# Kernel tuning notes

Hardware: AMD Instinct MI355X
Metric: run time of the kernel (lower is better)

## Reference

```python
import jax, jax.numpy as jnp
import numpy as np

B, H, W = 8, 512, 512
KSIZE = 11   # HVS Gaussian kernel size
SIGMA = 2.0
EPS = 1e-8


def _gauss_kernel():
    ax = jnp.arange(KSIZE, dtype=jnp.float32) - (KSIZE - 1) / 2.0
    g = jnp.exp(-(ax ** 2) / (2.0 * SIGMA ** 2))
    k = jnp.outer(g, g)
    return k / jnp.sum(k)


def _conv_same(x, k):
    # x: (B,1,H,W), k: (kh,kw) symmetric -> conv == correlation
    return jax.lax.conv_general_dilated(
        x, k[None, None, :, :], window_strides=(1, 1), padding='SAME',
        dimension_numbers=('NCHW', 'OIHW', 'NCHW'))


def setup_inputs() -> dict:
    key = jax.random.key(0)
    k1, k2, k3 = jax.random.split(key, 3)
    prob_map = jax.random.uniform(k1, (B, 1, H, W), dtype=jnp.float32,
                                  minval=0.01, maxval=0.99)
    c = jax.random.uniform(k2, (B, 1, H, W), dtype=jnp.float32)
    # binary halftone sampled per-pixel from prob_map
    h_sampled = (jax.random.uniform(k3, (B, 1, H, W)) < prob_map).astype(jnp.float32)
    return {"prob_map": prob_map, "c": c, "h_sampled": h_sampled}


def reference(prob_map, c, h_sampled):
    k = _gauss_kernel()
    # perceived error of the sampled halftone: e = G*h - c
    e = _conv_same(h_sampled, k) - c                     # (B,1,H,W)
    corr = _conv_same(e, k)                              # (G*e), G symmetric
    sum_k2 = jnp.sum(k * k)
    delta = 1.0 - 2.0 * h_sampled                        # flip change per pixel
    # reward_calc.compute_reward_with_flip, vectorized over all pixels:
    # E(flip at a) - E = 2*delta_a*(G*e)(a) + delta_a^2 * sum(G^2)
    reward = 2.0 * delta * corr + (delta ** 2) * sum_k2  # >0 means flip hurts
    log_prob = jnp.where(h_sampled > 0.5,
                         jnp.log(prob_map + EPS),
                         jnp.log(1.0 - prob_map + EPS))
    # local expected-gradient (REINFORCE) loss, averaged over batch
    loss = -jnp.sum(reward * log_prob) / prob_map.shape[0]
    return loss
```

## Files before the change

kernel.cpp:

```cpp
#include <hip/hip_runtime.h>

typedef float v2f __attribute__((ext_vector_type(2)));
typedef float v4f __attribute__((ext_vector_type(4)));

#define IMG 512
#define TS  32
#define TPB 2
#define NBLK 1024

#define A_STR  58
#define BT_STR 46
#define ET_STR 44
#define CT_STR 36

__device__ __forceinline__ v2f lo2(v4f v) { return __builtin_shufflevector(v, v, 0, 1); }
__device__ __forceinline__ v2f hi2(v4f v) { return __builtin_shufflevector(v, v, 2, 3); }

__device__ __forceinline__ v4f ldq(const float* __restrict__ hmap, size_t base,
                                   int x0, int y0, int idx) {
    int r = idx / 14, q = idx - r * 14;
    int gy = y0 - 10 + r, gx0 = x0 - 12 + 4 * q;
    v4f v = {0.f, 0.f, 0.f, 0.f};
    if ((unsigned)gy < IMG) {
        const float* hr = &hmap[base + ((size_t)gy << 9)];
        if (gx0 >= 0 && gx0 + 3 < IMG) {
            v = *(const v4f*)&hr[gx0];
        } else {
            if ((unsigned)(gx0 + 0) < IMG) v.x = hr[gx0 + 0];
            if ((unsigned)(gx0 + 1) < IMG) v.y = hr[gx0 + 1];
            if ((unsigned)(gx0 + 2) < IMG) v.z = hr[gx0 + 2];
            if ((unsigned)(gx0 + 3) < IMG) v.w = hr[gx0 + 3];
        }
    }
    return v;
}

__global__ __launch_bounds__(256, 4) void marl_fused(
    const float* __restrict__ prob,
    const float* __restrict__ cmap,
    const float* __restrict__ hmap,
    float* __restrict__ out)
{
    __shared__ __align__(16) float Abuf[52 * A_STR];
    __shared__ __align__(16) float Bbuf[56 * BT_STR];
    __shared__ float red[4];

    const float W[11] = {0.00881223f, 0.02714358f, 0.06511405f, 0.12164908f,
                         0.17699840f, 0.20056540f, 0.17699840f, 0.12164908f,
                         0.06511405f, 0.02714358f, 0.00881223f};
    v2f wv[11];
#pragma unroll
    for (int i = 0; i < 11; ++i) wv[i] = (v2f){W[i], W[i]};
    float w2 = 0.f;
#pragma unroll
    for (int i = 0; i < 11; ++i) w2 += W[i] * W[i];
    const float sumk2 = w2 * w2;
    const v2f z = {0.f, 0.f};

    const int tid = threadIdx.x;
    const int i0 = tid, i1 = tid + 256, i2 = tid + 512;
    const int T0 = blockIdx.x * TPB;

    const int p1run = tid % 7, p1q = tid / 7;
    const int p2p = tid % 21, p2eq = tid / 21;
    const int p3oyq = tid & 3, p3ex = tid >> 2;
    const int oy0e = 2 * (tid & 15), ox0 = 2 * (tid >> 4);

    v2f hv[TPB][2], pv[TPB][2];
    float creg[TPB][2][4];

    {
        const int b = T0 >> 8, r8 = T0 & 255;
        const int x0 = (r8 & 15) * TS, y0 = (r8 >> 4) * TS;
        const size_t base = (size_t)b << 18;
        v4f ha = ldq(hmap, base, x0, y0, i0);
        v4f hb = ldq(hmap, base, x0, y0, i1);
        v4f hc = (tid < 216) ? ldq(hmap, base, x0, y0, i2) : (v4f){0.f,0.f,0.f,0.f};
        if (tid < 231) {
#pragma unroll
            for (int h = 0; h < 2; ++h) {
                int gy = y0 - 5 + 2 * p2p + h;
#pragma unroll
                for (int c = 0; c < 4; ++c) {
                    int gx = x0 - 5 + 4 * p2eq + c;
                    creg[0][h][c] = ((unsigned)gy < IMG && (unsigned)gx < IMG)
                        ? cmap[base + ((size_t)gy << 9) + gx] : 0.f;
                }
            }
        }
#pragma unroll
        for (int h = 0; h < 2; ++h) {
            size_t rowb = base + ((size_t)(y0 + oy0e + h) << 9) + (x0 + ox0);
            hv[0][h] = *(const v2f*)&hmap[rowb];
            pv[0][h] = *(const v2f*)&prob[rowb];
        }
        { int r = i0 / 14, q = i0 - r * 14; *(v4f*)&Abuf[r * A_STR + 4 * q] = ha; }
        { int r = i1 / 14, q = i1 - r * 14; *(v4f*)&Abuf[r * A_STR + 4 * q] = hb; }
        if (tid < 216) { int r = i2 / 14, q = i2 - r * 14; *(v4f*)&Abuf[r * A_STR + 4 * q] = hc; }
    }
    __syncthreads();

    float partial = 0.f;
    v4f pfh0, pfh1, pfh2;

#pragma unroll
    for (int t = 0; t < TPB; ++t) {
        const int T = T0 + t;
        const int r8 = T & 255;
        const int x0 = (r8 & 15) * TS, y0 = (r8 >> 4) * TS;

        if (tid < 98) {
            int by0 = 6 * p1run;
            v2f accLo[6] = {z, z, z, z, z, z}, accHi[6] = {z, z, z, z, z, z};
#pragma unroll
            for (int i = 0; i < 16; ++i) {
                v4f a = *(const v4f*)&Abuf[(by0 + i) * A_STR + 4 * p1q];
                v2f lo = lo2(a), hi = hi2(a);
#pragma unroll
                for (int r = 0; r < 6; ++r) {
                    int j = i - r;
                    if (j >= 0 && j < 11) { accLo[r] += wv[j] * lo; accHi[r] += wv[j] * hi; }
                }
            }
#pragma unroll
            for (int r = 0; r < 6; ++r) {
                int by = by0 + r;
                Bbuf[(4 * p1q + 0) * BT_STR + by] = accLo[r].x;
                Bbuf[(4 * p1q + 1) * BT_STR + by] = accLo[r].y;
                Bbuf[(4 * p1q + 2) * BT_STR + by] = accHi[r].x;
                Bbuf[(4 * p1q + 3) * BT_STR + by] = accHi[r].y;
            }
        }
        __syncthreads();

        if (tid < 231) {
            int ex0 = 4 * p2eq, ey0 = 2 * p2p;
            v2f acc[4] = {z, z, z, z};
#pragma unroll
            for (int i = 0; i < 14; ++i) {
                v2f bb = *(const v2f*)&Bbuf[(ex0 + 2 + i) * BT_STR + ey0];
#pragma unroll
                for (int c = 0; c < 4; ++c) {
                    int j = i - c;
                    if (j >= 0 && j < 11) acc[c] += wv[j] * bb;
                }
            }
#pragma unroll
            for (int c = 0; c < 4; ++c) {
                int ex = ex0 + c;
                if (ex < 42) {
                    int gx = x0 - 5 + ex;
                    bool xin = (unsigned)gx < IMG;
#pragma unroll
                    for (int h = 0; h < 2; ++h) {
                        int gy = y0 - 5 + ey0 + h;
                        float v = 0.f;
                        if (xin && (unsigned)gy < IMG)
                            v = acc[c][h] - creg[t][h][c];
                        Abuf[ex * ET_STR + ey0 + h] = v;
                    }
                }
            }
        }
        __syncthreads();

        if (t + 1 < TPB) {
            const int Tn = T + 1;
            const int nb = Tn >> 8, nr8 = Tn & 255;
            const int nx0 = (nr8 & 15) * TS, ny0 = (nr8 >> 4) * TS;
            const size_t nbase = (size_t)nb << 18;
            pfh0 = ldq(hmap, nbase, nx0, ny0, i0);
            pfh1 = ldq(hmap, nbase, nx0, ny0, i1);
            if (tid < 216) pfh2 = ldq(hmap, nbase, nx0, ny0, i2);
            if (tid < 231) {
#pragma unroll
                for (int h = 0; h < 2; ++h) {
                    int gy = ny0 - 5 + 2 * p2p + h;
#pragma unroll
                    for (int c = 0; c < 4; ++c) {
                        int gx = nx0 - 5 + 4 * p2eq + c;
                        creg[t + 1][h][c] = ((unsigned)gy < IMG && (unsigned)gx < IMG)
                            ? cmap[nbase + ((size_t)gy << 9) + gx] : 0.f;
                    }
                }
            }
#pragma unroll
            for (int h = 0; h < 2; ++h) {
                size_t rowb = nbase + ((size_t)(ny0 + oy0e + h) << 9) + (nx0 + ox0);
                hv[t + 1][h] = *(const v2f*)&hmap[rowb];
                pv[t + 1][h] = *(const v2f*)&prob[rowb];
            }
        }
        if (tid < 168) {
            int oy0 = 8 * p3oyq;
            const float* src = &Abuf[p3ex * ET_STR + oy0];
            v4f w0 = *(const v4f*)&src[0];
            v4f w1 = *(const v4f*)&src[4];
            v4f w2_ = *(const v4f*)&src[8];
            v4f w3 = *(const v4f*)&src[12];
            v4f w4 = *(const v4f*)&src[16];
            float win[20];
            *(v4f*)&win[0] = w0; *(v4f*)&win[4] = w1; *(v4f*)&win[8] = w2_;
            *(v4f*)&win[12] = w3; *(v4f*)&win[16] = w4;
            float o[8];
#pragma unroll
            for (int k = 0; k < 8; ++k) {
                float acc = 0.f;
#pragma unroll
                for (int j = 0; j < 11; ++j) acc += W[j] * win[k + j];
                o[k] = acc;
            }
            *(v4f*)&Bbuf[p3ex * CT_STR + oy0]     = (v4f){o[0], o[1], o[2], o[3]};
            *(v4f*)&Bbuf[p3ex * CT_STR + oy0 + 4] = (v4f){o[4], o[5], o[6], o[7]};
        }
        __syncthreads();

        if (t + 1 < TPB) {
            { int r = i0 / 14, q = i0 - r * 14; *(v4f*)&Abuf[r * A_STR + 4 * q] = pfh0; }
            { int r = i1 / 14, q = i1 - r * 14; *(v4f*)&Abuf[r * A_STR + 4 * q] = pfh1; }
            if (tid < 216) { int r = i2 / 14, q = i2 - r * 14; *(v4f*)&Abuf[r * A_STR + 4 * q] = pfh2; }
        }
        {
            v2f acc[2] = {z, z};
#pragma unroll
            for (int i = 0; i < 12; ++i) {
                v2f ct = *(const v2f*)&Bbuf[(ox0 + i) * CT_STR + oy0e];
#pragma unroll
                for (int c = 0; c < 2; ++c) {
                    int j = i - c;
                    if (j >= 0 && j < 11) acc[c] += wv[j] * ct;
                }
            }
#pragma unroll
            for (int h = 0; h < 2; ++h) {
#pragma unroll
                for (int c = 0; c < 2; ++c) {
                    float h_ = hv[t][h][c], p_ = pv[t][h][c];
                    float logp = __logf(h_ > 0.5f ? p_ + 1e-8f : 1.f - p_ + 1e-8f);
                    float delta = 1.f - 2.f * h_;
                    partial += (2.f * delta * acc[c][h] + sumk2) * logp;
                }
            }
        }
        __syncthreads();
    }

#pragma unroll
    for (int off = 32; off > 0; off >>= 1)
        partial += __shfl_down(partial, off, 64);
    if ((tid & 63) == 0) red[tid >> 6] = partial;
    __syncthreads();
    if (tid == 0) {
        float s = red[0] + red[1] + red[2] + red[3];
        atomicAdd(out, s * -0.125f);
    }
}

extern "C" void kernel_launch(void* const* d_in, const int* in_sizes, int n_in,
                              void* d_out, int out_size, void* d_ws, size_t ws_size,
                              hipStream_t stream) {
    const float* prob = (const float*)d_in[0];
    const float* cmap = (const float*)d_in[1];
    const float* hmap = (const float*)d_in[2];
    float* out = (float*)d_out;

    hipMemsetAsync(out, 0, sizeof(float), stream);

    marl_fused<<<dim3(NBLK), dim3(256), 0, stream>>>(prob, cmap, hmap, out);
}
```

Before: 91.07 us.

## Process one tile per block and drop cross-tile prefetch pipeline

Each block now handles a single 32x32 tile instead of two, doubling the grid to 2048 blocks. The software prefetch of the next tile's halo, c values and h/prob is removed, which cuts register pressure, and launch bounds are raised to 6 blocks per SM. The aim is to hide memory latency through more resident blocks rather than in-block prefetch. The cost is that each block's loads now sit on its critical path, and there are more atomics and more per-block setup.

```diff
diff --git a/kernel.cpp b/kernel.cpp
--- a/kernel.cpp
+++ b/kernel.cpp
@@ -5,8 +5,7 @@
 
 #define IMG 512
 #define TS  32
-#define TPB 2
-#define NBLK 1024
+#define NBLK 2048
 
 #define A_STR  58
 #define BT_STR 46
@@ -35,7 +34,7 @@
     return v;
 }
 
-__global__ __launch_bounds__(256, 4) void marl_fused(
+__global__ __launch_bounds__(256, 6) void marl_fused(
     const float* __restrict__ prob,
     const float* __restrict__ cmap,
     const float* __restrict__ hmap,
@@ -59,20 +58,20 @@
 
     const int tid = threadIdx.x;
     const int i0 = tid, i1 = tid + 256, i2 = tid + 512;
-    const int T0 = blockIdx.x * TPB;
+
+    const int T  = blockIdx.x;
+    const int b  = T >> 8, r8 = T & 255;
+    const int x0 = (r8 & 15) * TS, y0 = (r8 >> 4) * TS;
+    const size_t base = (size_t)b << 18;
 
     const int p1run = tid % 7, p1q = tid / 7;
     const int p2p = tid % 21, p2eq = tid / 21;
     const int p3oyq = tid & 3, p3ex = tid >> 2;
     const int oy0e = 2 * (tid & 15), ox0 = 2 * (tid >> 4);
 
-    v2f hv[TPB][2], pv[TPB][2];
-    float creg[TPB][2][4];
-
+    v2f hv[2], pv[2];
+    float creg[2][4];
     {
-        const int b = T0 >> 8, r8 = T0 & 255;
-        const int x0 = (r8 & 15) * TS, y0 = (r8 >> 4) * TS;
-        const size_t base = (size_t)b << 18;
         v4f ha = ldq(hmap, base, x0, y0, i0);
         v4f hb = ldq(hmap, base, x0, y0, i1);
         v4f hc = (tid < 216) ? ldq(hmap, base, x0, y0, i2) : (v4f){0.f,0.f,0.f,0.f};
@@ -83,7 +82,7 @@
 #pragma unroll
                 for (int c = 0; c < 4; ++c) {
                     int gx = x0 - 5 + 4 * p2eq + c;
-                    creg[0][h][c] = ((unsigned)gy < IMG && (unsigned)gx < IMG)
+                    creg[h][c] = ((unsigned)gy < IMG && (unsigned)gx < IMG)
                         ? cmap[base + ((size_t)gy << 9) + gx] : 0.f;
                 }
             }
@@ -91,8 +90,8 @@
 #pragma unroll
         for (int h = 0; h < 2; ++h) {
             size_t rowb = base + ((size_t)(y0 + oy0e + h) << 9) + (x0 + ox0);
-            hv[0][h] = *(const v2f*)&hmap[rowb];
-            pv[0][h] = *(const v2f*)&prob[rowb];
+            hv[h] = *(const v2f*)&hmap[rowb];
+            pv[h] = *(const v2f*)&prob[rowb];
         }
         { int r = i0 / 14, q = i0 - r * 14; *(v4f*)&Abuf[r * A_STR + 4 * q] = ha; }
         { int r = i1 / 14, q = i1 - r * 14; *(v4f*)&Abuf[r * A_STR + 4 * q] = hb; }
@@ -100,149 +99,107 @@
     }
     __syncthreads();
 
+    if (tid < 98) {
+        int by0 = 6 * p1run;
+        v2f accLo[6] = {z, z, z, z, z, z}, accHi[6] = {z, z, z, z, z, z};
+#pragma unroll
+        for (int i = 0; i < 16; ++i) {
+            v4f a = *(const v4f*)&Abuf[(by0 + i) * A_STR + 4 * p1q];
+            v2f lo = lo2(a), hi = hi2(a);
+#pragma unroll
+            for (int r = 0; r < 6; ++r) {
+                int j = i - r;
+                if (j >= 0 && j < 11) { accLo[r] += wv[j] * lo; accHi[r] += wv[j] * hi; }
+            }
+        }
+#pragma unroll
+        for (int r = 0; r < 6; ++r) {
+            int by = by0 + r;
+            Bbuf[(4 * p1q + 0) * BT_STR + by] = accLo[r].x;
+            Bbuf[(4 * p1q + 1) * BT_STR + by] = accLo[r].y;
+            Bbuf[(4 * p1q + 2) * BT_STR + by] = accHi[r].x;
+            Bbuf[(4 * p1q + 3) * BT_STR + by] = accHi[r].y;
+        }
+    }
+    __syncthreads();
+
+    if (tid < 231) {
+        int ex0 = 4 * p2eq, ey0 = 2 * p2p;
+        v2f acc[4] = {z, z, z, z};
+#pragma unroll
+        for (int i = 0; i < 14; ++i) {
+            v2f bb = *(const v2f*)&Bbuf[(ex0 + 2 + i) * BT_STR + ey0];
+#pragma unroll
+            for (int c = 0; c < 4; ++c) {
+                int j = i - c;
+                if (j >= 0 && j < 11) acc[c] += wv[j] * bb;
+            }
+        }
+#pragma unroll
+        for (int c = 0; c < 4; ++c) {
+            int ex = ex0 + c;
+            if (ex < 42) {
+                int gx = x0 - 5 + ex;
+                bool xin = (unsigned)gx < IMG;
+#pragma unroll
+                for (int h = 0; h < 2; ++h) {
+                    int gy = y0 - 5 + ey0 + h;
+                    float v = 0.f;
+                    if (xin && (unsigned)gy < IMG)
+                        v = acc[c][h] - creg[h][c];
+                    Abuf[ex * ET_STR + ey0 + h] = v;
+                }
+            }
+        }
+    }
+    __syncthreads();
+
+    if (tid < 168) {
+        int oy0 = 8 * p3oyq;
+        const float* src = &Abuf[p3ex * ET_STR + oy0];
+        v4f w0 = *(const v4f*)&src[0];
+        v4f w1 = *(const v4f*)&src[4];
+        v4f w2_ = *(const v4f*)&src[8];
+        v4f w3 = *(const v4f*)&src[12];
+        v4f w4 = *(const v4f*)&src[16];
+        float win[20];
+        *(v4f*)&win[0] = w0; *(v4f*)&win[4] = w1; *(v4f*)&win[8] = w2_;
+        *(v4f*)&win[12] = w3; *(v4f*)&win[16] = w4;
+        float o[8];
+#pragma unroll
+        for (int k = 0; k < 8; ++k) {
+            float acc = 0.f;
+#pragma unroll
+            for (int j = 0; j < 11; ++j) acc += W[j] * win[k + j];
+            o[k] = acc;
+        }
+        *(v4f*)&Bbuf[p3ex * CT_STR + oy0]     = (v4f){o[0], o[1], o[2], o[3]};
+        *(v4f*)&Bbuf[p3ex * CT_STR + oy0 + 4] = (v4f){o[4], o[5], o[6], o[7]};
+    }
+    __syncthreads();
+
     float partial = 0.f;
-    v4f pfh0, pfh1, pfh2;
-
-#pragma unroll
-    for (int t = 0; t < TPB; ++t) {
-        const int T = T0 + t;
-        const int r8 = T & 255;
-        const int x0 = (r8 & 15) * TS, y0 = (r8 >> 4) * TS;
-
-        if (tid < 98) {
-            int by0 = 6 * p1run;
-            v2f accLo[6] = {z, z, z, z, z, z}, accHi[6] = {z, z, z, z, z, z};
-#pragma unroll
-            for (int i = 0; i < 16; ++i) {
-                v4f a = *(const v4f*)&Abuf[(by0 + i) * A_STR + 4 * p1q];
-                v2f lo = lo2(a), hi = hi2(a);
-#pragma unroll
-                for (int r = 0; r < 6; ++r) {
-                    int j = i - r;
-                    if (j >= 0 && j < 11) { accLo[r] += wv[j] * lo; accHi[r] += wv[j] * hi; }
-                }
-            }
-#pragma unroll
-            for (int r = 0; r < 6; ++r) {
-                int by = by0 + r;
-                Bbuf[(4 * p1q + 0) * BT_STR + by] = accLo[r].x;
-                Bbuf[(4 * p1q + 1) * BT_STR + by] = accLo[r].y;
-                Bbuf[(4 * p1q + 2) * BT_STR + by] = accHi[r].x;
-                Bbuf[(4 * p1q + 3) * BT_STR + by] = accHi[r].y;
-            }
-        }
-        __syncthreads();
-
-        if (tid < 231) {
-            int ex0 = 4 * p2eq, ey0 = 2 * p2p;
-            v2f acc[4] = {z, z, z, z};
-#pragma unroll
-            for (int i = 0; i < 14; ++i) {
-                v2f bb = *(const v2f*)&Bbuf[(ex0 + 2 + i) * BT_STR + ey0];
-#pragma unroll
-                for (int c = 0; c < 4; ++c) {
-                    int j = i - c;
-                    if (j >= 0 && j < 11) acc[c] += wv[j] * bb;
-                }
-            }
-#pragma unroll
-            for (int c = 0; c < 4; ++c) {
-                int ex = ex0 + c;
-                if (ex < 42) {
-                    int gx = x0 - 5 + ex;
-                    bool xin = (unsigned)gx < IMG;
-#pragma unroll
-                    for (int h = 0; h < 2; ++h) {
-                        int gy = y0 - 5 + ey0 + h;
-                        float v = 0.f;
-                        if (xin && (unsigned)gy < IMG)
-                            v = acc[c][h] - creg[t][h][c];
-                        Abuf[ex * ET_STR + ey0 + h] = v;
-                    }
-                }
-            }
-        }
-        __syncthreads();
-
-        if (t + 1 < TPB) {
-            const int Tn = T + 1;
-            const int nb = Tn >> 8, nr8 = Tn & 255;
-            const int nx0 = (nr8 & 15) * TS, ny0 = (nr8 >> 4) * TS;
-            const size_t nbase = (size_t)nb << 18;
-            pfh0 = ldq(hmap, nbase, nx0, ny0, i0);
-            pfh1 = ldq(hmap, nbase, nx0, ny0, i1);
-            if (tid < 216) pfh2 = ldq(hmap, nbase, nx0, ny0, i2);
-            if (tid < 231) {
-#pragma unroll
-                for (int h = 0; h < 2; ++h) {
-                    int gy = ny0 - 5 + 2 * p2p + h;
-#pragma unroll
-                    for (int c = 0; c < 4; ++c) {
-                        int gx = nx0 - 5 + 4 * p2eq + c;
-                        creg[t + 1][h][c] = ((unsigned)gy < IMG && (unsigned)gx < IMG)
-                            ? cmap[nbase + ((size_t)gy << 9) + gx] : 0.f;
-                    }
-                }
-            }
-#pragma unroll
-            for (int h = 0; h < 2; ++h) {
-                size_t rowb = nbase + ((size_t)(ny0 + oy0e + h) << 9) + (nx0 + ox0);
-                hv[t + 1][h] = *(const v2f*)&hmap[rowb];
-                pv[t + 1][h] = *(const v2f*)&prob[rowb];
-            }
-        }
-        if (tid < 168) {
-            int oy0 = 8 * p3oyq;
-            const float* src = &Abuf[p3ex * ET_STR + oy0];
-            v4f w0 = *(const v4f*)&src[0];
-            v4f w1 = *(const v4f*)&src[4];
-            v4f w2_ = *(const v4f*)&src[8];
-            v4f w3 = *(const v4f*)&src[12];
-            v4f w4 = *(const v4f*)&src[16];
-            float win[20];
-            *(v4f*)&win[0] = w0; *(v4f*)&win[4] = w1; *(v4f*)&win[8] = w2_;
-            *(v4f*)&win[12] = w3; *(v4f*)&win[16] = w4;
-            float o[8];
-#pragma unroll
-            for (int k = 0; k < 8; ++k) {
-                float acc = 0.f;
-#pragma unroll
-                for (int j = 0; j < 11; ++j) acc += W[j] * win[k + j];
-                o[k] = acc;
-            }
-            *(v4f*)&Bbuf[p3ex * CT_STR + oy0]     = (v4f){o[0], o[1], o[2], o[3]};
-            *(v4f*)&Bbuf[p3ex * CT_STR + oy0 + 4] = (v4f){o[4], o[5], o[6], o[7]};
-        }
-        __syncthreads();
-
-        if (t + 1 < TPB) {
-            { int r = i0 / 14, q = i0 - r * 14; *(v4f*)&Abuf[r * A_STR + 4 * q] = pfh0; }
-            { int r = i1 / 14, q = i1 - r * 14; *(v4f*)&Abuf[r * A_STR + 4 * q] = pfh1; }
-            if (tid < 216) { int r = i2 / 14, q = i2 - r * 14; *(v4f*)&Abuf[r * A_STR + 4 * q] = pfh2; }
-        }
-        {
-            v2f acc[2] = {z, z};
-#pragma unroll
-            for (int i = 0; i < 12; ++i) {
-                v2f ct = *(const v2f*)&Bbuf[(ox0 + i) * CT_STR + oy0e];
-#pragma unroll
-                for (int c = 0; c < 2; ++c) {
-                    int j = i - c;
-                    if (j >= 0 && j < 11) acc[c] += wv[j] * ct;
-                }
-            }
-#pragma unroll
-            for (int h = 0; h < 2; ++h) {
-#pragma unroll
-                for (int c = 0; c < 2; ++c) {
-                    float h_ = hv[t][h][c], p_ = pv[t][h][c];
-                    float logp = __logf(h_ > 0.5f ? p_ + 1e-8f : 1.f - p_ + 1e-8f);
-                    float delta = 1.f - 2.f * h_;
-                    partial += (2.f * delta * acc[c][h] + sumk2) * logp;
-                }
-            }
-        }
-        __syncthreads();
+    {
+        v2f acc[2] = {z, z};
+#pragma unroll
+        for (int i = 0; i < 12; ++i) {
+            v2f ct = *(const v2f*)&Bbuf[(ox0 + i) * CT_STR + oy0e];
+#pragma unroll
+            for (int c = 0; c < 2; ++c) {
+                int j = i - c;
+                if (j >= 0 && j < 11) acc[c] += wv[j] * ct;
+            }
+        }
+#pragma unroll
+        for (int h = 0; h < 2; ++h) {
+#pragma unroll
+            for (int c = 0; c < 2; ++c) {
+                float h_ = hv[h][c], p_ = pv[h][c];
+                float logp = __logf(h_ > 0.5f ? p_ + 1e-8f : 1.f - p_ + 1e-8f);
+                float delta = 1.f - 2.f * h_;
+                partial += (2.f * delta * acc[c][h] + sumk2) * logp;
+            }
+        }
     }
 
 #pragma unroll
```

Result: slower. 103.1 us (+13.2%).
